# Kernel tuning notes

Measured on AMD Instinct MI355X. Metric: run time of the kernel, lower is better.

## Reference

```python
import jax, jax.numpy as jnp
import numpy as np

USER_NUM = 100000
ITEM_NUM = 150000
N_NODES = USER_NUM + ITEM_NUM
EMB = 64
N_LAYERS = 3
N_EDGES = 1200000


def setup_inputs() -> dict:
    key = jax.random.key(0)
    k1, k2, k3, k4, k5 = jax.random.split(key, 5)
    user_emb = jax.random.normal(k1, (USER_NUM, EMB), dtype=jnp.float32) * 0.1
    item_emb = jax.random.normal(k2, (ITEM_NUM, EMB), dtype=jnp.float32) * 0.1
    adj_rows = jax.random.randint(k3, (N_EDGES,), 0, N_NODES, dtype=jnp.int32)
    adj_cols = jax.random.randint(k4, (N_EDGES,), 0, N_NODES, dtype=jnp.int32)
    # normalized-adjacency-like positive values
    adj_vals = jax.random.uniform(k5, (N_EDGES,), dtype=jnp.float32) * 0.1
    return {"user_emb": user_emb, "item_emb": item_emb,
            "adj_rows": adj_rows, "adj_cols": adj_cols, "adj_vals": adj_vals}


def _spmm(rows, cols, vals, embeds):
    # out[r] += vals[e] * embeds[cols[e]]  — torch.spmm(adj, embeds) with COO adj
    msgs = vals[:, None] * embeds[cols]           # [E, d]
    return jax.ops.segment_sum(msgs, rows, num_segments=N_NODES)


def reference(user_emb, item_emb, adj_rows, adj_cols, adj_vals):
    # forward_graphcl: concat embeddings, n_layers spmm hops, sum all hop outputs
    embeds = jnp.concatenate([user_emb, item_emb], axis=0)  # [N, d]
    main = embeds
    cur = embeds
    for _ in range(N_LAYERS):
        cur = _spmm(adj_rows, adj_cols, adj_vals, cur)
        main = main + cur
    return main
```

## Files before the change

kernel.cpp:

```cpp
#include <hip/hip_runtime.h>
#include <hip/hip_fp16.h>

#define USER_NUM 100000
#define ITEM_NUM 150000
#define N_NODES  250000
#define EMB      64
#define N_EDGES  1200000
#define N_ELEM   (N_NODES * EMB)

#define NBLK1 512
#define NBUCK 245
#define CAP   8192
#define TB1   4096
#define INIT_BLOCKS 3907

typedef float f4 __attribute__((ext_vector_type(4)));
typedef int   i4 __attribute__((ext_vector_type(4)));

__global__ __launch_bounds__(256) void bin_init_kernel(
    const int* __restrict__ rows, const int* __restrict__ cols,
    const float* __restrict__ vals,
    int* __restrict__ chunkcur, int* __restrict__ bucket_cnt,
    int2* __restrict__ tmp,
    const float* __restrict__ user, const float* __restrict__ item,
    __half* __restrict__ emb16)
{
    __shared__ int  scnt[256];
    __shared__ int  spref[256];
    __shared__ int  schunk[NBUCK];
    __shared__ unsigned char sbuck[TB1];
    __shared__ int2 tilebuf[TB1];

    int t = threadIdx.x;

    if (blockIdx.x >= NBLK1) {
        int gi = (blockIdx.x - NBLK1) * 256 + t;
        if (gi < N_ELEM / 16) {
            int base = gi * 16;
            const int UE = USER_NUM * EMB;
            const f4* src = (base < UE) ? (const f4*)(user + base)
                                        : (const f4*)(item + (base - UE));
            f4 f0 = __builtin_nontemporal_load(src);
            f4 f1 = __builtin_nontemporal_load(src + 1);
            f4 f2 = __builtin_nontemporal_load(src + 2);
            f4 f3 = __builtin_nontemporal_load(src + 3);
            union { i4 v; __half2 h[4]; } a, b;
            a.h[0] = __float22half2_rn(make_float2(f0.x, f0.y));
            a.h[1] = __float22half2_rn(make_float2(f0.z, f0.w));
            a.h[2] = __float22half2_rn(make_float2(f1.x, f1.y));
            a.h[3] = __float22half2_rn(make_float2(f1.z, f1.w));
            b.h[0] = __float22half2_rn(make_float2(f2.x, f2.y));
            b.h[1] = __float22half2_rn(make_float2(f2.z, f2.w));
            b.h[2] = __float22half2_rn(make_float2(f3.x, f3.y));
            b.h[3] = __float22half2_rn(make_float2(f3.z, f3.w));
            ((i4*)(emb16 + base))[0] = a.v;
            ((i4*)(emb16 + base))[1] = b.v;
        }
        return;
    }

    int b = blockIdx.x;
    int e0 = (int)((long long)b * N_EDGES / NBLK1);
    int e1 = (int)((long long)(b + 1) * N_EDGES / NBLK1);

    scnt[t] = 0;
    __syncthreads();
    for (int e = e0 + t; e < e1; e += 256)
        atomicAdd(&scnt[rows[e] >> 10], 1);
    __syncthreads();
    int realc = (t < NBUCK) ? scnt[t] : 0;
    int v     = (realc + 7) & ~7;
    __syncthreads();
    spref[t] = v;
    __syncthreads();
    for (int off = 1; off < 256; off <<= 1) {
        int u = (t >= off) ? spref[t - off] : 0;
        __syncthreads();
        spref[t] += u;
        __syncthreads();
    }
    int excl = spref[t] - v;
    __syncthreads();
    spref[t] = excl;
    __syncthreads();
    int padded_total = spref[NBUCK];

    scnt[t] = excl;
    if (t < NBUCK) {
        schunk[t] = (v > 0) ? atomicAdd(&chunkcur[t], v >> 3) : 0;
        if (realc > 0) atomicAdd(&bucket_cnt[t], realc);
        for (int k = realc; k < v; ++k) tilebuf[excl + k] = make_int2(-1, 0);
        for (int k = 0; k < v; ++k) sbuck[excl + k] = (unsigned char)t;
    }
    __syncthreads();
    for (int e = e0 + t; e < e1; e += 256) {
        int r  = rows[e];
        int lp = atomicAdd(&scnt[r >> 10], 1);
        tilebuf[lp] = make_int2(((r & 1023) << 18) | cols[e], __float_as_int(vals[e]));
    }
    __syncthreads();
    for (int j = t; j < padded_total; j += 256) {
        int lo = sbuck[j];
        tmp[(size_t)lo * CAP + schunk[lo] * 8 + (j - spref[lo])] = tilebuf[j];
    }
}

__global__ __launch_bounds__(256) void place_kernel(
    const int* __restrict__ chunkcur, const int* __restrict__ bucket_cnt,
    const int2* __restrict__ tmp,
    int* __restrict__ row_ptr, int2* __restrict__ edges)
{
    __shared__ int  shist[1024];
    __shared__ int  swave[256];
    __shared__ int  sbase[2];
    __shared__ int2 sstage[CAP];

    int t = threadIdx.x;
    int b = blockIdx.x;

    int vv = (t < NBUCK) ? bucket_cnt[t] : 0;
    swave[t] = vv;
    __syncthreads();
    for (int off = 1; off < 256; off <<= 1) {
        int u = (t >= off) ? swave[t - off] : 0;
        __syncthreads();
        swave[t] += u;
        __syncthreads();
    }
    if (t == 0) {
        sbase[0] = (b == 0) ? 0 : swave[b - 1];
        sbase[1] = swave[b];
        if (b == 0) row_ptr[N_NODES] = N_EDGES;
    }
    __syncthreads();
    int bb  = sbase[0];
    int cnt = sbase[1] - sbase[0];

    int nrec = chunkcur[b] * 8;
    const int2* src = tmp + (size_t)b * CAP;

    for (int i = t; i < 1024; i += 256) shist[i] = 0;
    __syncthreads();
    for (int j = t; j < nrec; j += 256) {
        int x = src[j].x;
        if (x != -1) atomicAdd(&shist[x >> 18], 1);
    }
    __syncthreads();
    int h0 = shist[4 * t], h1 = shist[4 * t + 1], h2 = shist[4 * t + 2], h3 = shist[4 * t + 3];
    int sum = h0 + h1 + h2 + h3;
    swave[t] = sum;
    __syncthreads();
    for (int off = 1; off < 256; off <<= 1) {
        int u = (t >= off) ? swave[t - off] : 0;
        __syncthreads();
        swave[t] += u;
        __syncthreads();
    }
    int base = swave[t] - sum;
    __syncthreads();
    shist[4 * t]     = base;
    shist[4 * t + 1] = base + h0;
    shist[4 * t + 2] = base + h0 + h1;
    shist[4 * t + 3] = base + h0 + h1 + h2;
    __syncthreads();
    for (int i = t; i < 1024; i += 256) {
        int idx = b * 1024 + i;
        if (idx < N_NODES) row_ptr[idx] = bb + shist[i];
    }
    __syncthreads();
    for (int j = t; j < nrec; j += 256) {
        int2 rec = src[j];
        if (rec.x != -1) {
            int lp = atomicAdd(&shist[rec.x >> 18], 1);
            sstage[lp] = make_int2(rec.x & 0x3FFFF, rec.y);
        }
    }
    __syncthreads();
    for (int j = t; j < cnt; j += 256)
        edges[bb + j] = sstage[j];
}

template <int MODE>
__global__ __launch_bounds__(256) void spmm_kernel(
    const int* __restrict__ row_ptr, const int2* __restrict__ edges,
    const __half* __restrict__ in16, const __half* __restrict__ emb16,
    const __half* __restrict__ cur1,
    float* __restrict__ out, __half* __restrict__ cur_out)
{
    int t = blockIdx.x * blockDim.x + threadIdx.x;
    int r = t >> 4;
    int l = t & 15;
    if (r >= N_NODES) return;
    int start = row_ptr[r];
    int end   = row_ptr[r + 1];
    int idx   = r * EMB + 4 * l;

    union { int2 i; __half2 h[2]; } pe, p1, p2;
    if (MODE == 1) {
        pe.i = *(const int2*)(emb16 + idx);
        p1.i = *(const int2*)(cur1 + idx);
        p2.i = *(const int2*)(in16 + idx);
    }

    float ax = 0.f, ay = 0.f, az = 0.f, aw = 0.f;
    for (int j = start; j < end; j += 8) {
        int2 e[8];
#pragma unroll
        for (int k = 0; k < 8; ++k) e[k] = edges[j + k];
#pragma unroll
        for (int k = 0; k < 8; ++k) {
            bool ok = (j + k < end);
            int   c = ok ? e[k].x : 0;
            float v = ok ? __int_as_float(e[k].y) : 0.0f;
            union { int2 i; __half2 h[2]; } g;
            g.i = *(const int2*)(in16 + c * EMB + 4 * l);
            float2 x0 = __half22float2(g.h[0]);
            float2 x1 = __half22float2(g.h[1]);
            ax += v * x0.x; ay += v * x0.y;
            az += v * x1.x; aw += v * x1.y;
        }
    }

    if (MODE == 0) {
        union { int2 i; __half2 h[2]; } o;
        o.h[0] = __float22half2_rn(make_float2(ax, ay));
        o.h[1] = __float22half2_rn(make_float2(az, aw));
        *(int2*)(cur_out + idx) = o.i;
    } else {
        float2 e0 = __half22float2(pe.h[0]), e1 = __half22float2(pe.h[1]);
        float2 c0 = __half22float2(p1.h[0]), c1 = __half22float2(p1.h[1]);
        float2 d0 = __half22float2(p2.h[0]), d1 = __half22float2(p2.h[1]);
        float4 o = make_float4(e0.x + c0.x + d0.x + ax,
                               e0.y + c0.y + d0.y + ay,
                               e1.x + c1.x + d1.x + az,
                               e1.y + c1.y + d1.y + aw);
        *(float4*)(out + idx) = o;
    }
}

extern "C" void kernel_launch(void* const* d_in, const int* in_sizes, int n_in,
                              void* d_out, int out_size, void* d_ws, size_t ws_size,
                              hipStream_t stream) {
    const float* user = (const float*)d_in[0];
    const float* item = (const float*)d_in[1];
    const int*   rows = (const int*)d_in[2];
    const int*   cols = (const int*)d_in[3];
    const float* vals = (const float*)d_in[4];
    float*       out  = (float*)d_out;

    char* p = (char*)d_ws;
    __half* emb16    = (__half*)p;  p += (size_t)N_ELEM * 2;
    __half* cur1     = (__half*)p;  p += (size_t)N_ELEM * 2;
    __half* cur2     = (__half*)p;  p += (size_t)N_ELEM * 2;
    int2*   tmp      = (int2*)p;    p += (size_t)NBUCK * CAP * 8;
    int2*   edges    = (int2*)p;    p += (size_t)N_EDGES * 8 + 256;
    int*    row_ptr  = (int*)p;     p += 1000448;
    int*    bucket_base = (int*)p;  p += 1024;
    int*    bucket_cnt  = (int*)p;  p += 1024;
    int*    chunkcur    = (int*)p;  p += 1024;

    hipMemsetAsync(bucket_cnt, 0, 2048, stream);

    bin_init_kernel<<<NBLK1 + INIT_BLOCKS, 256, 0, stream>>>(
        rows, cols, vals, chunkcur, bucket_cnt, tmp, user, item, emb16);
    place_kernel<<<NBUCK, 256, 0, stream>>>(chunkcur, bucket_cnt, tmp, row_ptr, edges);

    const int spmm_blocks = (N_NODES * 16 + 255) / 256;
    spmm_kernel<0><<<spmm_blocks, 256, 0, stream>>>(row_ptr, edges, emb16, emb16, cur1, out, cur1);
    spmm_kernel<0><<<spmm_blocks, 256, 0, stream>>>(row_ptr, edges, cur1, emb16, cur1, out, cur2);
    spmm_kernel<1><<<spmm_blocks, 256, 0, stream>>>(row_ptr, edges, cur2, emb16, cur1, out, nullptr);
}
```

Before: 279.8 us.

## Replace bucketed two-pass binning with global-atomic counting sort for CSR build

```diff
diff --git a/kernel.cpp b/kernel.cpp
--- a/kernel.cpp
+++ b/kernel.cpp
@@ -8,33 +8,24 @@
 #define N_EDGES  1200000
 #define N_ELEM   (N_NODES * EMB)
 
-#define NBLK1 512
-#define NBUCK 245
-#define CAP   8192
-#define TB1   4096
+#define NBLK_E 512
+#define NBUCK  245
 #define INIT_BLOCKS 3907
+#define ROW_PAD 250944
 
 typedef float f4 __attribute__((ext_vector_type(4)));
 typedef int   i4 __attribute__((ext_vector_type(4)));
 
-__global__ __launch_bounds__(256) void bin_init_kernel(
-    const int* __restrict__ rows, const int* __restrict__ cols,
-    const float* __restrict__ vals,
-    int* __restrict__ chunkcur, int* __restrict__ bucket_cnt,
-    int2* __restrict__ tmp,
+__global__ __launch_bounds__(256) void hist_init_kernel(
+    const int* __restrict__ rows,
+    int* __restrict__ row_cnt, int* __restrict__ bucket_cnt,
     const float* __restrict__ user, const float* __restrict__ item,
     __half* __restrict__ emb16)
 {
-    __shared__ int  scnt[256];
-    __shared__ int  spref[256];
-    __shared__ int  schunk[NBUCK];
-    __shared__ unsigned char sbuck[TB1];
-    __shared__ int2 tilebuf[TB1];
-
     int t = threadIdx.x;
 
-    if (blockIdx.x >= NBLK1) {
-        int gi = (blockIdx.x - NBLK1) * 256 + t;
+    if (blockIdx.x >= NBLK_E) {
+        int gi = (blockIdx.x - NBLK_E) * 256 + t;
         if (gi < N_ELEM / 16) {
             int base = gi * 16;
             const int UE = USER_NUM * EMB;
@@ -59,125 +50,77 @@
         return;
     }
 
-    int b = blockIdx.x;
-    int e0 = (int)((long long)b * N_EDGES / NBLK1);
-    int e1 = (int)((long long)(b + 1) * N_EDGES / NBLK1);
+    __shared__ int scnt[256];
+    int b  = blockIdx.x;
+    int e0 = (int)((long long)b * N_EDGES / NBLK_E);
+    int e1 = (int)((long long)(b + 1) * N_EDGES / NBLK_E);
 
     scnt[t] = 0;
     __syncthreads();
-    for (int e = e0 + t; e < e1; e += 256)
-        atomicAdd(&scnt[rows[e] >> 10], 1);
-    __syncthreads();
-    int realc = (t < NBUCK) ? scnt[t] : 0;
-    int v     = (realc + 7) & ~7;
-    __syncthreads();
-    spref[t] = v;
+    for (int e = e0 + t; e < e1; e += 256) {
+        int r = rows[e];
+        atomicAdd(&row_cnt[r], 1);
+        atomicAdd(&scnt[r >> 10], 1);
+    }
+    __syncthreads();
+    if (t < NBUCK && scnt[t] > 0) atomicAdd(&bucket_cnt[t], scnt[t]);
+}
+
+__global__ __launch_bounds__(256) void scan_kernel(
+    const int* __restrict__ bucket_cnt,
+    int* __restrict__ row_cnt,
+    int* __restrict__ row_ptr)
+{
+    __shared__ int sb[256];
+    __shared__ int sw[256];
+    int t = threadIdx.x, b = blockIdx.x;
+
+    int v = (t < NBUCK) ? bucket_cnt[t] : 0;
+    sb[t] = v;
     __syncthreads();
     for (int off = 1; off < 256; off <<= 1) {
-        int u = (t >= off) ? spref[t - off] : 0;
-        __syncthreads();
-        spref[t] += u;
-        __syncthreads();
-    }
-    int excl = spref[t] - v;
-    __syncthreads();
-    spref[t] = excl;
-    __syncthreads();
-    int padded_total = spref[NBUCK];
-
-    scnt[t] = excl;
-    if (t < NBUCK) {
-        schunk[t] = (v > 0) ? atomicAdd(&chunkcur[t], v >> 3) : 0;
-        if (realc > 0) atomicAdd(&bucket_cnt[t], realc);
-        for (int k = realc; k < v; ++k) tilebuf[excl + k] = make_int2(-1, 0);
-        for (int k = 0; k < v; ++k) sbuck[excl + k] = (unsigned char)t;
-    }
-    __syncthreads();
-    for (int e = e0 + t; e < e1; e += 256) {
-        int r  = rows[e];
-        int lp = atomicAdd(&scnt[r >> 10], 1);
-        tilebuf[lp] = make_int2(((r & 1023) << 18) | cols[e], __float_as_int(vals[e]));
-    }
-    __syncthreads();
-    for (int j = t; j < padded_total; j += 256) {
-        int lo = sbuck[j];
-        tmp[(size_t)lo * CAP + schunk[lo] * 8 + (j - spref[lo])] = tilebuf[j];
-    }
-}
-
-__global__ __launch_bounds__(256) void place_kernel(
-    const int* __restrict__ chunkcur, const int* __restrict__ bucket_cnt,
-    const int2* __restrict__ tmp,
-    int* __restrict__ row_ptr, int2* __restrict__ edges)
-{
-    __shared__ int  shist[1024];
-    __shared__ int  swave[256];
-    __shared__ int  sbase[2];
-    __shared__ int2 sstage[CAP];
-
-    int t = threadIdx.x;
-    int b = blockIdx.x;
-
-    int vv = (t < NBUCK) ? bucket_cnt[t] : 0;
-    swave[t] = vv;
+        int u = (t >= off) ? sb[t - off] : 0;
+        __syncthreads();
+        sb[t] += u;
+        __syncthreads();
+    }
+    int bbase = (b == 0) ? 0 : sb[b - 1];
+
+    int i0 = b * 1024 + 4 * t;
+    i4 c = *(const i4*)(row_cnt + i0);
+    int sum = c.x + c.y + c.z + c.w;
+    sw[t] = sum;
     __syncthreads();
     for (int off = 1; off < 256; off <<= 1) {
-        int u = (t >= off) ? swave[t - off] : 0;
-        __syncthreads();
-        swave[t] += u;
-        __syncthreads();
-    }
-    if (t == 0) {
-        sbase[0] = (b == 0) ? 0 : swave[b - 1];
-        sbase[1] = swave[b];
-        if (b == 0) row_ptr[N_NODES] = N_EDGES;
-    }
-    __syncthreads();
-    int bb  = sbase[0];
-    int cnt = sbase[1] - sbase[0];
-
-    int nrec = chunkcur[b] * 8;
-    const int2* src = tmp + (size_t)b * CAP;
-
-    for (int i = t; i < 1024; i += 256) shist[i] = 0;
-    __syncthreads();
-    for (int j = t; j < nrec; j += 256) {
-        int x = src[j].x;
-        if (x != -1) atomicAdd(&shist[x >> 18], 1);
-    }
-    __syncthreads();
-    int h0 = shist[4 * t], h1 = shist[4 * t + 1], h2 = shist[4 * t + 2], h3 = shist[4 * t + 3];
-    int sum = h0 + h1 + h2 + h3;
-    swave[t] = sum;
-    __syncthreads();
-    for (int off = 1; off < 256; off <<= 1) {
-        int u = (t >= off) ? swave[t - off] : 0;
-        __syncthreads();
-        swave[t] += u;
-        __syncthreads();
-    }
-    int base = swave[t] - sum;
-    __syncthreads();
-    shist[4 * t]     = base;
-    shist[4 * t + 1] = base + h0;
-    shist[4 * t + 2] = base + h0 + h1;
-    shist[4 * t + 3] = base + h0 + h1 + h2;
-    __syncthreads();
-    for (int i = t; i < 1024; i += 256) {
-        int idx = b * 1024 + i;
-        if (idx < N_NODES) row_ptr[idx] = bb + shist[i];
-    }
-    __syncthreads();
-    for (int j = t; j < nrec; j += 256) {
-        int2 rec = src[j];
-        if (rec.x != -1) {
-            int lp = atomicAdd(&shist[rec.x >> 18], 1);
-            sstage[lp] = make_int2(rec.x & 0x3FFFF, rec.y);
-        }
-    }
-    __syncthreads();
-    for (int j = t; j < cnt; j += 256)
-        edges[bb + j] = sstage[j];
+        int u = (t >= off) ? sw[t - off] : 0;
+        __syncthreads();
+        sw[t] += u;
+        __syncthreads();
+    }
+    int base = bbase + sw[t] - sum;
+
+    i4 o;
+    o.x = base;
+    o.y = base + c.x;
+    o.z = base + c.x + c.y;
+    o.w = base + c.x + c.y + c.z;
+    *(i4*)(row_ptr + i0) = o;
+    *(i4*)(row_cnt + i0) = o;
+}
+
+__global__ __launch_bounds__(256) void scatter_kernel(
+    const int* __restrict__ rows, const int* __restrict__ cols,
+    const float* __restrict__ vals,
+    int* __restrict__ cursor, int2* __restrict__ edges)
+{
+    int e = blockIdx.x * 256 + threadIdx.x;
+    if (e < N_EDGES) {
+        int r    = rows[e];
+        int cv   = cols[e];
+        float vv = vals[e];
+        int slot = atomicAdd(&cursor[r], 1);
+        edges[slot] = make_int2(cv, __float_as_int(vv));
+    }
 }
 
 template <int MODE>
@@ -249,21 +192,21 @@
     float*       out  = (float*)d_out;
 
     char* p = (char*)d_ws;
-    __half* emb16    = (__half*)p;  p += (size_t)N_ELEM * 2;
-    __half* cur1     = (__half*)p;  p += (size_t)N_ELEM * 2;
-    __half* cur2     = (__half*)p;  p += (size_t)N_ELEM * 2;
-    int2*   tmp      = (int2*)p;    p += (size_t)NBUCK * CAP * 8;
-    int2*   edges    = (int2*)p;    p += (size_t)N_EDGES * 8 + 256;
-    int*    row_ptr  = (int*)p;     p += 1000448;
-    int*    bucket_base = (int*)p;  p += 1024;
-    int*    bucket_cnt  = (int*)p;  p += 1024;
-    int*    chunkcur    = (int*)p;  p += 1024;
-
-    hipMemsetAsync(bucket_cnt, 0, 2048, stream);
-
-    bin_init_kernel<<<NBLK1 + INIT_BLOCKS, 256, 0, stream>>>(
-        rows, cols, vals, chunkcur, bucket_cnt, tmp, user, item, emb16);
-    place_kernel<<<NBUCK, 256, 0, stream>>>(chunkcur, bucket_cnt, tmp, row_ptr, edges);
+    __half* emb16   = (__half*)p;  p += (size_t)N_ELEM * 2;
+    __half* cur1    = (__half*)p;  p += (size_t)N_ELEM * 2;
+    __half* cur2    = (__half*)p;  p += (size_t)N_ELEM * 2;
+    int2*   edges   = (int2*)p;    p += (size_t)(N_EDGES + 32) * 8;
+    int*    row_ptr = (int*)p;     p += (size_t)ROW_PAD * 4;
+    int*    row_cnt = (int*)p;     p += (size_t)ROW_PAD * 4;
+    int*    bucket_cnt = (int*)p;  p += 4096;
+
+    hipMemsetAsync(row_cnt, 0, (size_t)ROW_PAD * 4 + 4096, stream);
+
+    hist_init_kernel<<<NBLK_E + INIT_BLOCKS, 256, 0, stream>>>(
+        rows, row_cnt, bucket_cnt, user, item, emb16);
+    scan_kernel<<<NBUCK, 256, 0, stream>>>(bucket_cnt, row_cnt, row_ptr);
+    scatter_kernel<<<(N_EDGES + 255) / 256, 256, 0, stream>>>(
+        rows, cols, vals, row_cnt, edges);
 
     const int spmm_blocks = (N_NODES * 16 + 255) / 256;
     spmm_kernel<0><<<spmm_blocks, 256, 0, stream>>>(row_ptr, edges, emb16, emb16, cur1, out, cur1);
```

Measured after the change: 361.7 us. +29.3%, slower.

## Split CSR placement kernel into four sub-blocks per bucket

Applied to the files above, without the earlier changes.

```diff
diff --git a/kernel.cpp b/kernel.cpp
--- a/kernel.cpp
+++ b/kernel.cpp
@@ -12,7 +12,8 @@
 #define NBUCK 245
 #define CAP   8192
 #define TB1   4096
-#define INIT_BLOCKS 3907
+#define INIT_TILES 3907
+#define SST   2048
 
 typedef float f4 __attribute__((ext_vector_type(4)));
 typedef int   i4 __attribute__((ext_vector_type(4)));
@@ -90,7 +91,7 @@
         schunk[t] = (v > 0) ? atomicAdd(&chunkcur[t], v >> 3) : 0;
         if (realc > 0) atomicAdd(&bucket_cnt[t], realc);
         for (int k = realc; k < v; ++k) tilebuf[excl + k] = make_int2(-1, 0);
-        for (int k = 0; k < v; ++k) sbuck[excl + k] = (unsigned char)t;
+        for (int k = 0; k < v; ++k)     sbuck[excl + k] = (unsigned char)t;
     }
     __syncthreads();
     for (int e = e0 + t; e < e1; e += 256) {
@@ -105,18 +106,18 @@
     }
 }
 
-__global__ __launch_bounds__(256) void place_kernel(
+__global__ __launch_bounds__(256) void place4_kernel(
     const int* __restrict__ chunkcur, const int* __restrict__ bucket_cnt,
     const int2* __restrict__ tmp,
     int* __restrict__ row_ptr, int2* __restrict__ edges)
 {
     __shared__ int  shist[1024];
     __shared__ int  swave[256];
-    __shared__ int  sbase[2];
-    __shared__ int2 sstage[CAP];
+    __shared__ int2 sstage[SST];
 
     int t = threadIdx.x;
-    int b = blockIdx.x;
+    int b = blockIdx.x >> 2;
+    int s = blockIdx.x & 3;
 
     int vv = (t < NBUCK) ? bucket_cnt[t] : 0;
     swave[t] = vv;
@@ -127,26 +128,23 @@
         swave[t] += u;
         __syncthreads();
     }
-    if (t == 0) {
-        sbase[0] = (b == 0) ? 0 : swave[b - 1];
-        sbase[1] = swave[b];
-        if (b == 0) row_ptr[N_NODES] = N_EDGES;
-    }
-    __syncthreads();
-    int bb  = sbase[0];
-    int cnt = sbase[1] - sbase[0];
+    int bb  = (b == 0) ? 0 : swave[b - 1];
+    int cnt = swave[b] - bb;
+    __syncthreads();
+
+    for (int i = t; i < 1024; i += 256) shist[i] = 0;
+    __syncthreads();
 
     int nrec = chunkcur[b] * 8;
     const int2* src = tmp + (size_t)b * CAP;
-
-    for (int i = t; i < 1024; i += 256) shist[i] = 0;
-    __syncthreads();
     for (int j = t; j < nrec; j += 256) {
         int x = src[j].x;
         if (x != -1) atomicAdd(&shist[x >> 18], 1);
     }
     __syncthreads();
-    int h0 = shist[4 * t], h1 = shist[4 * t + 1], h2 = shist[4 * t + 2], h3 = shist[4 * t + 3];
+
+    int h0 = shist[4 * t], h1 = shist[4 * t + 1];
+    int h2 = shist[4 * t + 2], h3 = shist[4 * t + 3];
     int sum = h0 + h1 + h2 + h3;
     swave[t] = sum;
     __syncthreads();
@@ -156,28 +154,34 @@
         swave[t] += u;
         __syncthreads();
     }
-    int base = swave[t] - sum;
+    int base = bb + swave[t] - sum;
     __syncthreads();
     shist[4 * t]     = base;
     shist[4 * t + 1] = base + h0;
     shist[4 * t + 2] = base + h0 + h1;
     shist[4 * t + 3] = base + h0 + h1 + h2;
     __syncthreads();
-    for (int i = t; i < 1024; i += 256) {
-        int idx = b * 1024 + i;
-        if (idx < N_NODES) row_ptr[idx] = bb + shist[i];
-    }
-    __syncthreads();
+
+    int wstart = shist[s * 256];
+    int wend   = (s < 3) ? shist[(s + 1) * 256] : bb + cnt;
+    {
+        int idx = b * 1024 + s * 256 + t;
+        if (idx < N_NODES) row_ptr[idx] = shist[s * 256 + t];
+    }
+    if (blockIdx.x == 0 && t == 0) row_ptr[N_NODES] = N_EDGES;
+    __syncthreads();
+
     for (int j = t; j < nrec; j += 256) {
         int2 rec = src[j];
-        if (rec.x != -1) {
-            int lp = atomicAdd(&shist[rec.x >> 18], 1);
+        int  rl  = rec.x >> 18;
+        if (rec.x != -1 && (rl >> 8) == s) {
+            int lp = atomicAdd(&shist[rl], 1) - wstart;
             sstage[lp] = make_int2(rec.x & 0x3FFFF, rec.y);
         }
     }
     __syncthreads();
-    for (int j = t; j < cnt; j += 256)
-        edges[bb + j] = sstage[j];
+    for (int j = t; j < wend - wstart; j += 256)
+        edges[wstart + j] = sstage[j];
 }
 
 template <int MODE>
@@ -249,21 +253,21 @@
     float*       out  = (float*)d_out;
 
     char* p = (char*)d_ws;
-    __half* emb16    = (__half*)p;  p += (size_t)N_ELEM * 2;
-    __half* cur1     = (__half*)p;  p += (size_t)N_ELEM * 2;
-    __half* cur2     = (__half*)p;  p += (size_t)N_ELEM * 2;
-    int2*   tmp      = (int2*)p;    p += (size_t)NBUCK * CAP * 8;
-    int2*   edges    = (int2*)p;    p += (size_t)N_EDGES * 8 + 256;
-    int*    row_ptr  = (int*)p;     p += 1000448;
-    int*    bucket_base = (int*)p;  p += 1024;
-    int*    bucket_cnt  = (int*)p;  p += 1024;
-    int*    chunkcur    = (int*)p;  p += 1024;
+    __half* emb16   = (__half*)p;  p += (size_t)N_ELEM * 2;
+    __half* cur1    = (__half*)p;  p += (size_t)N_ELEM * 2;
+    __half* cur2    = (__half*)p;  p += (size_t)N_ELEM * 2;
+    int2*   tmp     = (int2*)p;    p += (size_t)NBUCK * CAP * 8;
+    int2*   edges   = (int2*)p;    p += (size_t)(N_EDGES + 32) * 8;
+    int*    row_ptr = (int*)p;     p += 1000448;
+    int*    bucket_cnt = (int*)p;  p += 1024;
+    int*    chunkcur   = (int*)p;  p += 1024;
 
     hipMemsetAsync(bucket_cnt, 0, 2048, stream);
 
-    bin_init_kernel<<<NBLK1 + INIT_BLOCKS, 256, 0, stream>>>(
+    bin_init_kernel<<<NBLK1 + INIT_TILES, 256, 0, stream>>>(
         rows, cols, vals, chunkcur, bucket_cnt, tmp, user, item, emb16);
-    place_kernel<<<NBUCK, 256, 0, stream>>>(chunkcur, bucket_cnt, tmp, row_ptr, edges);
+    place4_kernel<<<NBUCK * 4, 256, 0, stream>>>(
+        chunkcur, bucket_cnt, tmp, row_ptr, edges);
 
     const int spmm_blocks = (N_NODES * 16 + 255) / 256;
     spmm_kernel<0><<<spmm_blocks, 256, 0, stream>>>(row_ptr, edges, emb16, emb16, cur1, out, cur1);
```

Result: slower. 286.7 us (+2.5%).
